# Kernel optimization log

Measured on AMD Instinct MI355X. Metric: run time of the kernel, lower is better.

The kernel has to match this reference:

```python
import jax, jax.numpy as jnp
import numpy as np

B, H, W = 8, 1024, 1024

SOBEL_X = jnp.array([[-1, 0, 1], [-2, 0, 2], [-1, 0, 1]], jnp.float32).reshape(1, 1, 3, 3)
SOBEL_Y = jnp.array([[-1, -2, -1], [0, 0, 0], [1, 2, 1]], jnp.float32).reshape(1, 1, 3, 3)
LAPLACIAN = jnp.array([[0, -1, 0], [-1, 4, -1], [0, -1, 0]], jnp.float32).reshape(1, 1, 3, 3)
TWO_PI = 2.0 * np.pi


def _conv(x, k, pad):
    return jax.lax.conv_general_dilated(
        x, k, window_strides=(1, 1), padding=[(pad, pad), (pad, pad)],
        dimension_numbers=('NCHW', 'OIHW', 'NCHW'))


def _boundary_mask(mask, w):
    ks = 2 * w + 1
    kernel = jnp.ones((1, 1, ks, ks), jnp.float32)
    s = _conv(mask, kernel, w)
    dilated = (s > 0).astype(jnp.float32)
    eroded = (s >= float(ks * ks)).astype(jnp.float32)
    return jnp.clip(dilated - eroded, 0.0, 1.0)


def _elev_grads(e):
    gx = _conv(e, SOBEL_X, 1)
    gy = _conv(e, SOBEL_Y, 1)
    mag = jnp.sqrt(gx * gx + gy * gy + 1e-8)
    dirn = jnp.arctan2(gy, gx + 1e-8)
    curv = _conv(e, LAPLACIAN, 1)
    return mag, dirn, curv


def _high_freq_mask(h, w):
    ii, jj = jnp.meshgrid(jnp.arange(h, dtype=jnp.float32), jnp.arange(w, dtype=jnp.float32), indexing='ij')
    dist = jnp.sqrt((ii - h // 2) ** 2 + (jj - w // 2) ** 2)
    return (dist > min(h, w) * 0.3).astype(jnp.float32).reshape(1, 1, h, w)


def setup_inputs() -> dict:
    key = jax.random.key(0)
    k1, k2, k3 = jax.random.split(key, 3)
    pred = jax.random.normal(k1, (B, 1, H, W), jnp.float32)
    target = jax.random.normal(k2, (B, 1, H, W), jnp.float32)
    mask = jax.random.randint(k3, (B, 1, H, W), 0, 2).astype(jnp.float32)
    return {'pred_elevation': pred, 'target_elevation': target, 'mask': mask}


def reference(pred_elevation, target_elevation, mask):
    # boundary masks for widths 1..3
    bms = [_boundary_mask(mask, w) for w in (1, 2, 3)]

    # ---- gradient continuity loss ----
    p_mag, p_dir, p_curv = _elev_grads(pred_elevation)
    t_mag, t_dir, t_curv = _elev_grads(target_elevation)
    slope_diff = jnp.abs(p_mag - t_mag)
    dir_diff = jnp.abs(p_dir - t_dir)
    dir_diff = jnp.minimum(dir_diff, TWO_PI - dir_diff)
    curv_diff = jnp.abs(p_curv - t_curv)
    grad_loss = 0.0
    for i, bm in enumerate(bms):
        w_sd = 1.0 if i == 0 else 0.5
        w_cv = 2.0 if i == 0 else 1.0
        grad_loss = grad_loss + w_sd * jnp.mean(slope_diff * bm)
        grad_loss = grad_loss + w_sd * jnp.mean(dir_diff * bm)
        grad_loss = grad_loss + w_cv * jnp.mean(curv_diff * bm)
    grad_loss = grad_loss / len(bms)

    # ---- frequency continuity loss ----
    pf = jnp.fft.fft2(pred_elevation)
    tf = jnp.fft.fft2(target_elevation)
    p_magf, t_magf = jnp.abs(pf), jnp.abs(tf)
    p_ph = jnp.arctan2(pf.imag, pf.real)
    t_ph = jnp.arctan2(tf.imag, tf.real)
    hf = _high_freq_mask(H, W)
    mag_loss = jnp.mean((p_magf * hf - t_magf * hf) ** 2)
    d = p_ph - t_ph
    phase_diff = jnp.arctan2(jnp.sin(d), jnp.cos(d))  # wrap to (-pi, pi]
    phase_loss = jnp.mean((phase_diff * hf) ** 2)
    freq_loss = mag_loss + 2.0 * phase_loss

    # ---- smoothness constraint (width_1 only) ----
    kern9 = jnp.ones((1, 1, 3, 3), jnp.float32) / 9.0
    local_mean = _conv(pred_elevation, kern9, 1)
    local_mean_sq = _conv(pred_elevation ** 2, kern9, 1)
    local_var = jnp.clip(local_mean_sq - local_mean ** 2, 1e-8, None)
    local_std = jnp.sqrt(local_var)
    smooth_loss = jnp.mean(local_std * bms[0])

    # ---- slope continuity (width_1 only) ----
    psx = _conv(p_mag, SOBEL_X, 1)
    psy = _conv(p_mag, SOBEL_Y, 1)
    p_change = jnp.sqrt(psx ** 2 + psy ** 2 + 1e-8)
    tsx = _conv(t_mag, SOBEL_X, 1)
    tsy = _conv(t_mag, SOBEL_Y, 1)
    t_change = jnp.sqrt(tsx ** 2 + tsy ** 2 + 1e-8)
    slope_loss = jnp.mean(jnp.abs(p_change - t_change) * bms[0])

    total = 2.0 * grad_loss + 1.5 * freq_loss + 3.0 * smooth_loss + 2.0 * slope_loss
    return (total, grad_loss, freq_loss, smooth_loss, slope_loss)
```

## Files before the change

### kernel.cpp

```cpp
#include <hip/hip_runtime.h>

#define HW 1024
#define TWO_PI_F 6.28318530717958647692f
#define NSLOT 64

typedef float v2f __attribute__((ext_vector_type(2)));
typedef int   i2v __attribute__((ext_vector_type(2)));

__device__ __forceinline__ v2f mkv2(float a, float b){ v2f r; r.x = a; r.y = b; return r; }
__device__ __forceinline__ v2f v2s(float s){ v2f r; r.x = s; r.y = s; return r; }

__device__ __forceinline__ float2 cmulf(float2 a, float2 b){
  return make_float2(a.x*b.x - a.y*b.y, a.x*b.y + a.y*b.x);
}
__device__ __forceinline__ float fsqrt(float x){ return __builtin_amdgcn_sqrtf(x); }

__device__ __forceinline__ float fast_atan2_abs(float ay, float x){
  float ax = fabsf(x);
  float mx = fmaxf(ax, ay), mn = fminf(ax, ay);
  float a  = mn * __builtin_amdgcn_rcpf(fmaxf(mx, 1e-37f));
  float s  = a * a;
  float r  = ((((0.0208351f*s - 0.085133f)*s + 0.180141f)*s - 0.3302995f)*s
              + 0.999866f) * a;
  r = (ay > ax) ? 1.57079632679f - r : r;
  return (x < 0.f) ? 3.14159265359f - r : r;
}

__device__ __forceinline__ float block_reduce_add_f(float v, float* sc){
  int tid = threadIdx.x;
  #pragma unroll
  for (int o = 32; o > 0; o >>= 1) v += __shfl_down(v, o, 64);
  __syncthreads();
  if ((tid & 63) == 0) sc[tid >> 6] = v;
  __syncthreads();
  return sc[0] + sc[1] + sc[2] + sc[3];
}

__global__ void setup_kernel(double* acc, float2* twg){
  int i = threadIdx.x + blockIdx.x * 256;
  if (i < 5 * NSLOT) acc[i] = 0.0;
  if (i < 512){
    float s, c; sincosf(-TWO_PI_F * (float)i * (1.f/1024.f), &s, &c);
    twg[i] = make_float2(c, s);
  }
}

template<int Z0>
__global__ __launch_bounds__(256, 4)
void spatial_kernel(const float* __restrict__ pred, const float* __restrict__ targ,
                    const float* __restrict__ mask, double* __restrict__ acc){
  __shared__ v2f spt[36*44];
  __shared__ v2f pmt[34*35];
  __shared__ unsigned long long mrow[38];
  __shared__ float sc[4];
  float* const smkf = (float*)pmt;

  const int tid = threadIdx.x;
  const int x0 = blockIdx.x << 5, y0 = blockIdx.y << 5;
  const int z = blockIdx.z + Z0;
  const size_t ib = (size_t)z * ((size_t)HW * HW);
  const bool interior = ((unsigned)(blockIdx.x - 1) < 30u) &&
                        ((unsigned)(blockIdx.y - 1) < 30u);

  if (interior){
    const float* pb = pred + ib;
    const float* tb = targ + ib;
    for (int i = tid; i < 360; i += 256){
      int a = i / 10, b = i % 10;
      size_t off = (size_t)(y0 - 2 + a) * HW + (x0 - 4 + 4*b);
      float4 pv = *(const float4*)(pb + off);
      float4 tv = *(const float4*)(tb + off);
      int o = a*44 + 4*b;
      spt[o+0] = mkv2(pv.x, tv.x);
      spt[o+1] = mkv2(pv.y, tv.y);
      spt[o+2] = mkv2(pv.z, tv.z);
      spt[o+3] = mkv2(pv.w, tv.w);
    }
    const float* mb = mask + ib;
    for (int i = tid; i < 380; i += 256){
      int a = i / 10, b = i % 10;
      size_t off = (size_t)(y0 - 3 + a) * HW + (x0 - 4 + 4*b);
      float4 v = *(const float4*)(mb + off);
      int o = a*41 + 4*b;
      smkf[o]=v.x; smkf[o+1]=v.y; smkf[o+2]=v.z; smkf[o+3]=v.w;
    }
  } else {
    for (int i = tid; i < 1296; i += 256){
      int a = i / 36, b = i % 36;
      int gy = y0 - 2 + a, gx = x0 - 2 + b;
      float pv = 0.f, tv = 0.f;
      if ((unsigned)gy < HW && (unsigned)gx < HW){
        size_t idx = ib + (size_t)gy * HW + gx;
        pv = pred[idx]; tv = targ[idx];
      }
      spt[a*44 + b + 2] = mkv2(pv, tv);
    }
    for (int i = tid; i < 1444; i += 256){
      int a = i / 38, b = i % 38;
      int gy = y0 - 3 + a, gx = x0 - 3 + b;
      float v = 0.f;
      if ((unsigned)gy < HW && (unsigned)gx < HW) v = mask[ib + (size_t)gy * HW + gx];
      smkf[a*41 + b + 1] = v;
    }
  }
  __syncthreads();

  {
    const int wv = tid >> 6, lane = tid & 63;
    for (int r = wv; r < 38; r += 4){
      float val = (lane < 38) ? smkf[r*41 + 1 + lane] : 0.f;
      unsigned long long m = __ballot(val > 0.5f);
      if (lane == 0) mrow[r] = m;
    }
  }
  __syncthreads();

  if (interior){
    for (int i = tid; i < 1156; i += 256){
      int iy = i / 34, ix = i % 34;
      int o = iy*44 + ix + 2;
      v2f a00=spt[o],    a01=spt[o+1],  a02=spt[o+2];
      v2f a10=spt[o+44],                a12=spt[o+46];
      v2f a20=spt[o+88], a21=spt[o+89], a22=spt[o+90];
      v2f gx = (a02 + v2s(2.f)*a12 + a22) - (a00 + v2s(2.f)*a10 + a20);
      v2f gy = (a20 + v2s(2.f)*a21 + a22) - (a00 + v2s(2.f)*a01 + a02);
      v2f m2 = gx*gx + gy*gy + v2s(1e-8f);
      pmt[iy*35+ix] = mkv2(fsqrt(m2.x), fsqrt(m2.y));
    }
  } else {
    for (int i = tid; i < 1156; i += 256){
      int iy = i / 34, ix = i % 34;
      int gy = y0 - 1 + iy, gx = x0 - 1 + ix;
      v2f out = v2s(0.f);
      if ((unsigned)gy < HW && (unsigned)gx < HW){
        int o = iy*44 + ix + 2;
        v2f a00=spt[o],    a01=spt[o+1],  a02=spt[o+2];
        v2f a10=spt[o+44],                a12=spt[o+46];
        v2f a20=spt[o+88], a21=spt[o+89], a22=spt[o+90];
        v2f gxv = (a02 + v2s(2.f)*a12 + a22) - (a00 + v2s(2.f)*a10 + a20);
        v2f gyv = (a20 + v2s(2.f)*a21 + a22) - (a00 + v2s(2.f)*a01 + a02);
        v2f m2 = gxv*gxv + gyv*gyv + v2s(1e-8f);
        out = mkv2(fsqrt(m2.x), fsqrt(m2.y));
      }
      pmt[iy*35+ix] = out;
    }
  }
  __syncthreads();

  const int ty = tid >> 5, tx = tid & 31;
  const int r0 = ty << 2;

  int cp[10];
  #pragma unroll
  for (int j = 0; j < 10; j++){
    unsigned w = (unsigned)(mrow[r0 + j] >> tx);
    int c3 = __popc(w & 0x7Fu);
    int c2 = __popc((w >> 1) & 0x1Fu);
    int c1 = __popc((w >> 2) & 0x7u);
    cp[j] = c1 | (c2 << 8) | (c3 << 16);
  }

  v2f PQ[3][3], AB[3][3];
  #pragma unroll
  for (int rr = 0; rr < 2; rr++)
    #pragma unroll
    for (int cc = 0; cc < 3; cc++){
      PQ[rr][cc] = spt[(r0+1+rr)*44 + tx+3+cc];
      AB[rr][cc] = pmt[(r0+rr)*35 + tx+cc];
    }

  v2f wR[6], wA[6];
  float uR[6], qR[6];
  #pragma unroll
  for (int r = 0; r < 2; r++){
    wR[r] = PQ[r][0] + v2s(2.f)*PQ[r][1] + PQ[r][2];
    float p0 = PQ[r][0].x, p1 = PQ[r][1].x, p2 = PQ[r][2].x;
    uR[r] = p0 + p1 + p2;
    qR[r] = fmaf(p0, p0, fmaf(p1, p1, p2*p2));
    wA[r] = AB[r][0] + v2s(2.f)*AB[r][1] + AB[r][2];
  }

  float accg = 0.f, accs = 0.f, accl = 0.f;
  #pragma unroll
  for (int k = 0; k < 4; k++){
    #pragma unroll
    for (int cc = 0; cc < 3; cc++){
      PQ[2][cc] = spt[(r0+k+3)*44 + tx+3+cc];
      AB[2][cc] = pmt[(r0+k+2)*35 + tx+cc];
    }
    {
      wR[k+2] = PQ[2][0] + v2s(2.f)*PQ[2][1] + PQ[2][2];
      float p0 = PQ[2][0].x, p1 = PQ[2][1].x, p2 = PQ[2][2].x;
      uR[k+2] = p0 + p1 + p2;
      qR[k+2] = fmaf(p0, p0, fmaf(p1, p1, p2*p2));
      wA[k+2] = AB[2][0] + v2s(2.f)*AB[2][1] + AB[2][2];
    }

    v2f gxv = (PQ[0][2] + v2s(2.f)*PQ[1][2] + PQ[2][2]) - (PQ[0][0] + v2s(2.f)*PQ[1][0] + PQ[2][0]);
    v2f gyv = wR[k+2] - wR[k];
    v2f cvv = v2s(4.f)*PQ[1][1] - PQ[0][1] - PQ[1][0] - PQ[1][2] - PQ[2][1];

    float sd = fabsf(AB[1][1].x - AB[1][1].y);
    float x1 = gxv.x + 1e-8f, y1 = gyv.x;
    float x2 = gxv.y + 1e-8f, y2 = gyv.y;
    float dd = fast_atan2_abs(fabsf(y1*x2 - x1*y2), x1*x2 + y1*y2);
    float cd = fabsf(cvv.x - cvv.y);

    int s1p = cp[k+2] + cp[k+3] + cp[k+4];
    int s2p = s1p + cp[k+1] + cp[k+5];
    int s3p = s2p + cp[k]   + cp[k+6];
    int s1 = s1p & 0xFF;
    int s2 = (s2p >> 8) & 0xFF;
    int s3 = s3p >> 16;
    float w1 = ((unsigned)(s1 - 1) <  8u) ? 1.f : 0.f;
    float w2 = ((unsigned)(s2 - 1) < 24u) ? 1.f : 0.f;
    float w3 = ((unsigned)(s3 - 1) < 48u) ? 1.f : 0.f;
    float wa = fmaf(0.5f, w2 + w3, w1);

    accg = fmaf(wa, sd + dd + 2.f*cd, accg);

    float s9 = uR[k] + uR[k+1] + uR[k+2];
    float s9q = qR[k] + qR[k+1] + qR[k+2];
    float lm = s9 * (1.f/9.f), lq = s9q * (1.f/9.f);
    accs = fmaf(fsqrt(fmaxf(lq - lm*lm, 1e-8f)), w1, accs);

    v2f px = (AB[0][2] + v2s(2.f)*AB[1][2] + AB[2][2]) - (AB[0][0] + v2s(2.f)*AB[1][0] + AB[2][0]);
    v2f py = wA[k+2] - wA[k];
    v2f ch2 = px*px + py*py + v2s(1e-8f);
    accl = fmaf(fabsf(fsqrt(ch2.x) - fsqrt(ch2.y)), w1, accl);

    if (k < 3){
      #pragma unroll
      for (int cc = 0; cc < 3; cc++){
        PQ[0][cc] = PQ[1][cc]; PQ[1][cc] = PQ[2][cc];
        AB[0][cc] = AB[1][cc]; AB[1][cc] = AB[2][cc];
      }
    }
  }

  float g  = block_reduce_add_f(accg, sc);
  float sm = block_reduce_add_f(accs, sc);
  float sl = block_reduce_add_f(accl, sc);
  if (tid == 0){
    int slot = (blockIdx.x + blockIdx.y * 7 + z * 13) & (NSLOT - 1);
    atomicAdd(&acc[0*NSLOT + slot], (double)g);
    atomicAdd(&acc[1*NSLOT + slot], (double)sm);
    atomicAdd(&acc[2*NSLOT + slot], (double)sl);
  }
}

template<int CTRL>
__device__ __forceinline__ float xordpp(float x){
  int xi = __float_as_int(x);
  return __int_as_float(__builtin_amdgcn_update_dpp(xi, xi, CTRL, 0xF, 0xF, true));
}
__device__ __forceinline__ float xor4v(float x){
  int xi = __float_as_int(x);
  int t1 = __builtin_amdgcn_update_dpp(xi, xi, 0x104, 0xF, 0x5, false);
  int t2 = __builtin_amdgcn_update_dpp(t1, xi, 0x114, 0xF, 0xA, false);
  return __int_as_float(t2);
}

#define FC 0.70710678118654752f
#define FC1 0.92387953251128676f
#define FS1 0.38268343236508977f

__device__ __forceinline__ void bfly(float2& a, float2& b){
  float tx = b.x, ty = b.y;
  b.x = a.x - tx; b.y = a.y - ty;
  a.x += tx;      a.y += ty;
}
__device__ __forceinline__ void cmul_c(float2& b, float wr, float wi){
  float tx = wr*b.x - wi*b.y, ty = wr*b.y + wi*b.x;
  b.x = tx; b.y = ty;
}
__device__ __forceinline__ void rotmi(float2& b){
  float t = b.x; b.x = b.y; b.y = -t;
}

__device__ __forceinline__ void fft16_reg(float2* v){
  float2 y[16];
  y[0]=v[0];  y[1]=v[8];  y[2]=v[4];  y[3]=v[12];
  y[4]=v[2];  y[5]=v[10]; y[6]=v[6];  y[7]=v[14];
  y[8]=v[1];  y[9]=v[9];  y[10]=v[5]; y[11]=v[13];
  y[12]=v[3]; y[13]=v[11];y[14]=v[7]; y[15]=v[15];
  #pragma unroll
  for (int g = 0; g < 8; g++) bfly(y[2*g], y[2*g+1]);
  #pragma unroll
  for (int g = 0; g < 4; g++){
    int b = 4*g;
    bfly(y[b], y[b+2]);
    rotmi(y[b+3]); bfly(y[b+1], y[b+3]);
  }
  #pragma unroll
  for (int g = 0; g < 2; g++){
    int b = 8*g;
    bfly(y[b], y[b+4]);
    cmul_c(y[b+5],  FC, -FC); bfly(y[b+1], y[b+5]);
    rotmi(y[b+6]);            bfly(y[b+2], y[b+6]);
    cmul_c(y[b+7], -FC, -FC); bfly(y[b+3], y[b+7]);
  }
  bfly(y[0], y[8]);
  cmul_c(y[9],   FC1, -FS1); bfly(y[1], y[9]);
  cmul_c(y[10],  FC,  -FC);  bfly(y[2], y[10]);
  cmul_c(y[11],  FS1, -FC1); bfly(y[3], y[11]);
  rotmi(y[12]);              bfly(y[4], y[12]);
  cmul_c(y[13], -FS1, -FC1); bfly(y[5], y[13]);
  cmul_c(y[14], -FC,  -FC);  bfly(y[6], y[14]);
  cmul_c(y[15], -FC1, -FS1); bfly(y[7], y[15]);
  #pragma unroll
  for (int j = 0; j < 16; j++) v[j] = y[j];
}

__device__ __forceinline__ void fft1024_wave(float2* v, int lane ,
                                             const float2* __restrict__ twg){
  const float2 tw1 = twg[(lane & 1) << 8];
  const float2 tw2 = twg[(lane & 3) << 7];
  const float2 tw3 = twg[(lane & 7) << 6];
  const float2 tw4 = twg[(lane & 15) << 5];
  const float2 tw5 = twg[(lane & 31) << 4];
  const float2 wq  = twg[lane];

  {
    const float sgn = (lane & 1) ? -1.f : 1.f;
    #pragma unroll
    for (int j = 0; j < 16; j++){
      i2v px = __builtin_amdgcn_permlane32_swap(__float_as_int(v[j].x), __float_as_int(v[j].x), false, false);
      i2v py = __builtin_amdgcn_permlane32_swap(__float_as_int(v[j].y), __float_as_int(v[j].y), false, false);
      v[j].x = fmaf(sgn, __int_as_float(px.y), __int_as_float(px.x));
      v[j].y = fmaf(sgn, __int_as_float(py.y), __int_as_float(py.x));
    }
  }
  {
    const bool up = (lane & 2) != 0;
    const float ewx = up ? tw1.x : 1.f, ewy = up ? tw1.y : 0.f;
    const float sgn = up ? -1.f : 1.f;
    #pragma unroll
    for (int j = 0; j < 16; j++){
      float tx = ewx*v[j].x - ewy*v[j].y;
      float ty = ewx*v[j].y + ewy*v[j].x;
      i2v px = __builtin_amdgcn_permlane16_swap(__float_as_int(tx), __float_as_int(tx), false, false);
      i2v py = __builtin_amdgcn_permlane16_swap(__float_as_int(ty), __float_as_int(ty), false, false);
      v[j].x = fmaf(sgn, __int_as_float(px.y), __int_as_float(px.x));
      v[j].y = fmaf(sgn, __int_as_float(py.y), __int_as_float(py.x));
    }
  }
  {
    const bool up = (lane & 4) != 0;
    const float ewx = up ? tw2.x : 1.f, ewy = up ? tw2.y : 0.f;
    const float sgn = up ? -1.f : 1.f;
    #pragma unroll
    for (int j = 0; j < 16; j++){
      float tx = ewx*v[j].x - ewy*v[j].y;
      float ty = ewx*v[j].y + ewy*v[j].x;
      v[j].x = fmaf(sgn, tx, xordpp<0x128>(tx));
      v[j].y = fmaf(sgn, ty, xordpp<0x128>(ty));
    }
  }
  {
    const bool up = (lane & 8) != 0;
    const float ewx = up ? tw3.x : 1.f, ewy = up ? tw3.y : 0.f;
    const float sgn = up ? -1.f : 1.f;
    #pragma unroll
    for (int j = 0; j < 16; j++){
      float tx = ewx*v[j].x - ewy*v[j].y;
      float ty = ewx*v[j].y + ewy*v[j].x;
      v[j].x = fmaf(sgn, tx, xor4v(tx));
      v[j].y = fmaf(sgn, ty, xor4v(ty));
    }
  }
  {
    const bool up = (lane & 16) != 0;
    const float ewx = up ? tw4.x : 1.f, ewy = up ? tw4.y : 0.f;
    const float sgn = up ? -1.f : 1.f;
    #pragma unroll
    for (int j = 0; j < 16; j++){
      float tx = ewx*v[j].x - ewy*v[j].y;
      float ty = ewx*v[j].y + ewy*v[j].x;
      v[j].x = fmaf(sgn, tx, xordpp<0x4E>(tx));
      v[j].y = fmaf(sgn, ty, xordpp<0x4E>(ty));
    }
  }
  {
    const bool up = (lane & 32) != 0;
    const float ewx = up ? tw5.x : 1.f, ewy = up ? tw5.y : 0.f;
    const float sgn = up ? -1.f : 1.f;
    #pragma unroll
    for (int j = 0; j < 16; j++){
      float tx = ewx*v[j].x - ewy*v[j].y;
      float ty = ewx*v[j].y + ewy*v[j].x;
      v[j].x = fmaf(sgn, tx, xordpp<0xB1>(tx));
      v[j].y = fmaf(sgn, ty, xordpp<0xB1>(ty));
    }
  }
  float2 w2 = cmulf(wq, wq);
  float2 w3 = cmulf(w2, wq);
  float2 w4 = cmulf(w2, w2);
  float2 w5 = cmulf(w3, w2);
  float2 w6 = cmulf(w3, w3);
  float2 w7 = cmulf(w4, w3);
  float2 w8 = cmulf(w4, w4);
  v[1]  = cmulf(v[1],  wq);
  v[2]  = cmulf(v[2],  w2);
  v[3]  = cmulf(v[3],  w3);
  v[4]  = cmulf(v[4],  w4);
  v[5]  = cmulf(v[5],  w5);
  v[6]  = cmulf(v[6],  w6);
  v[7]  = cmulf(v[7],  w7);
  v[8]  = cmulf(v[8],  w8);
  v[9]  = cmulf(cmulf(v[9],  w8), wq);
  v[10] = cmulf(cmulf(v[10], w8), w2);
  v[11] = cmulf(cmulf(v[11], w8), w3);
  v[12] = cmulf(cmulf(v[12], w8), w4);
  v[13] = cmulf(cmulf(v[13], w8), w5);
  v[14] = cmulf(cmulf(v[14], w8), w6);
  v[15] = cmulf(cmulf(v[15], w8), w7);
  fft16_reg(v);
}

__global__ __launch_bounds__(512, 2)
void fft_rows_t_kernel(const float* __restrict__ pred, const float* __restrict__ targ,
                       float2* __restrict__ Zt, const float2* __restrict__ twg){
  __shared__ float2 tile[8][64][9];
  const int tid = threadIdx.x;
  const int lane = tid & 63;
  const int w = tid >> 6;
  const int y0 = blockIdx.x << 3;
  const size_t ibase = ((size_t)blockIdx.y * HW + (y0 + w)) * HW;
  const int rb = __brev(lane) >> 26;
  const float4* p4 = (const float4*)(pred + ibase);
  const float4* t4 = (const float4*)(targ + ibase);
  float2 v[16];
  #pragma unroll
  for (int m = 0; m < 4; m++){
    float4 a = p4[4*lane + m];
    float4 b = t4[4*lane + m];
    v[4*m+0] = make_float2(a.x, b.x);
    v[4*m+1] = make_float2(a.y, b.y);
    v[4*m+2] = make_float2(a.z, b.z);
    v[4*m+3] = make_float2(a.w, b.w);
  }
  fft1024_wave(v, rb, twg);
  float2* zb = Zt + (size_t)blockIdx.y * HW * HW + (size_t)blockIdx.x * 8192;
  const int yl = tid & 7, kl = tid >> 3;
  #pragma unroll
  for (int jb = 0; jb < 2; jb++){
    __syncthreads();
    #pragma unroll
    for (int jj = 0; jj < 8; jj++) tile[jj][lane][w] = v[8*jb + jj];
    __syncthreads();
    #pragma unroll
    for (int jj = 0; jj < 8; jj++){
      int k = ((jb << 3) + jj) * 64 + kl;
      zb[k * 8 + yl] = tile[jj][kl][yl];
    }
  }
}

__device__ __forceinline__ void freq_contrib(float2 Zk, float2 Zm, int k1, int k2,
                                             float& ms, float& ps){
  int di = k1 - 512, dj = k2 - 512;
  if (di*di + dj*dj < 94372) return;
  float pr = 0.5f*(Zk.x + Zm.x);
  float pi = 0.5f*(Zk.y - Zm.y);
  float tr = 0.5f*(Zk.y + Zm.y);
  float ti = 0.5f*(Zm.x - Zk.x);
  float p2 = pr*pr + pi*pi;
  float t2 = tr*tr + ti*ti;
  ms += p2 + t2 - 2.f*fsqrt(p2*t2);
  float re = pr*tr + pi*ti;
  float im = pi*tr - pr*ti;
  float pd = fast_atan2_abs(fabsf(im), re);
  ps += pd*pd;
}

__global__ __launch_bounds__(256, 2)
void fft_cols2_kernel(const float2* __restrict__ Z, const float2* __restrict__ twg,
                      double* __restrict__ acc){
  __shared__ float2 ex[4][1024];
  const int lane = threadIdx.x & 63;
  const int w = threadIdx.x >> 6;
  const int p = 2 * blockIdx.x + (w >> 1);
  const bool valid = (p <= 512);
  const int r_spec = (w & 1) ? ((1024 - p) & 1023) : p;
  const int rr = (r_spec & 0x3C0) | (__brev(r_spec & 63) >> 26);
  const float2* base = Z + (size_t)blockIdx.y * HW * HW;
  const int bl = __brev(lane) >> 26;

  float2 v[16];
  if (valid){
    const float4* f4 = (const float4*)base;
    #pragma unroll
    for (int s = 0; s < 2; s++){
      size_t o = (size_t)(2*lane + s) * 4096 + (size_t)rr * 4;
      #pragma unroll
      for (int q = 0; q < 4; q++){
        float4 x = f4[o + q];
        v[8*s + 2*q]     = make_float2(x.x, x.y);
        v[8*s + 2*q + 1] = make_float2(x.z, x.w);
      }
    }
    fft1024_wave(v, bl, twg);
    #pragma unroll
    for (int j = 0; j < 16; j++) ex[w][bl + (j << 6)] = v[j];
  }
  __syncthreads();
  if (!valid) return;
  const bool self = (p == 0) || (p == 512);
  if ((w & 1) && self) return;

  const float2* pb = ex[w ^ 1];
  float ms = 0.f, ps = 0.f;
  #pragma unroll
  for (int j = 0; j < 16; j++){
    int k = bl + (j << 6);
    float2 zm = pb[(1024 - k) & 1023];
    freq_contrib(v[j], zm, k, r_spec, ms, ps);
  }
  #pragma unroll
  for (int o = 32; o > 0; o >>= 1){
    ms += __shfl_down(ms, o, 64);
    ps += __shfl_down(ps, o, 64);
  }
  if (lane == 0){
    int slot = (r_spec + blockIdx.y * 11) & (NSLOT - 1);
    atomicAdd(&acc[3*NSLOT + slot], (double)ms);
    atomicAdd(&acc[4*NSLOT + slot], (double)ps);
  }
}

__global__ void finalize_kernel(const double* __restrict__ acc, float* __restrict__ out){
  const int t = threadIdx.x;
  double v[5];
  #pragma unroll
  for (int s = 0; s < 5; s++) v[s] = acc[s*NSLOT + t];
  #pragma unroll
  for (int o = 32; o > 0; o >>= 1)
    #pragma unroll
    for (int s = 0; s < 5; s++) v[s] += __shfl_down(v[s], o, 64);
  if (t == 0){
    const double inv = 1.0 / 8388608.0;
    double grad   = v[0] * inv / 3.0;
    double smooth = v[1] * inv;
    double slope  = v[2] * inv;
    double freq   = (v[3] + 2.0 * v[4]) * inv;
    double total  = 2.0*grad + 1.5*freq + 3.0*smooth + 2.0*slope;
    out[0] = (float)total;
    out[1] = (float)grad;
    out[2] = (float)freq;
    out[3] = (float)smooth;
    out[4] = (float)slope;
  }
}

extern "C" void kernel_launch(void* const* d_in, const int* in_sizes, int n_in,
                              void* d_out, int out_size, void* d_ws, size_t ws_size,
                              hipStream_t stream){
  const float* pred = (const float*)d_in[0];
  const float* targ = (const float*)d_in[1];
  const float* mask = (const float*)d_in[2];
  double* acc  = (double*)d_ws;
  float2* twg  = (float2*)((char*)d_ws + 4096);
  float2* Z    = (float2*)((char*)d_ws + 8192);

  setup_kernel<<<2, 256, 0, stream>>>(acc, twg);
  spatial_kernel<0><<<dim3(32, 32, 4), 256, 0, stream>>>(pred, targ, mask, acc);
  spatial_kernel<4><<<dim3(32, 32, 4), 256, 0, stream>>>(pred, targ, mask, acc);
  fft_rows_t_kernel<<<dim3(128, 8), 512, 0, stream>>>(pred, targ, Z, twg);
  fft_cols2_kernel<<<dim3(257, 8), 256, 0, stream>>>(Z, twg, acc);
  finalize_kernel<<<1, 64, 0, stream>>>(acc, (float*)d_out);
}
```

Measured before the change: 241.1 us.

## Drop setup kernel, compute twiddles inline, merge spatial launches

Removes the setup kernel: the accumulators are now zeroed with hipMemsetAsync and the FFT twiddles are computed per lane with sincosf instead of read from a global table. The two spatial_kernel launches (batches 0-3 and 4-7) become one launch over all 8 batches. The aim is fewer launches and fewer inter-kernel gaps, at the cost of extra transcendental math in each FFT wave.

```diff
diff --git a/kernel.cpp b/kernel.cpp
--- a/kernel.cpp
+++ b/kernel.cpp
@@ -36,16 +36,6 @@
   return sc[0] + sc[1] + sc[2] + sc[3];
 }
 
-__global__ void setup_kernel(double* acc, float2* twg){
-  int i = threadIdx.x + blockIdx.x * 256;
-  if (i < 5 * NSLOT) acc[i] = 0.0;
-  if (i < 512){
-    float s, c; sincosf(-TWO_PI_F * (float)i * (1.f/1024.f), &s, &c);
-    twg[i] = make_float2(c, s);
-  }
-}
-
-template<int Z0>
 __global__ __launch_bounds__(256, 4)
 void spatial_kernel(const float* __restrict__ pred, const float* __restrict__ targ,
                     const float* __restrict__ mask, double* __restrict__ acc){
@@ -57,7 +47,7 @@
 
   const int tid = threadIdx.x;
   const int x0 = blockIdx.x << 5, y0 = blockIdx.y << 5;
-  const int z = blockIdx.z + Z0;
+  const int z = blockIdx.z;
   const size_t ib = (size_t)z * ((size_t)HW * HW);
   const bool interior = ((unsigned)(blockIdx.x - 1) < 30u) &&
                         ((unsigned)(blockIdx.y - 1) < 30u);
@@ -312,14 +302,19 @@
   for (int j = 0; j < 16; j++) v[j] = y[j];
 }
 
-__device__ __forceinline__ void fft1024_wave(float2* v, int lane ,
-                                             const float2* __restrict__ twg){
-  const float2 tw1 = twg[(lane & 1) << 8];
-  const float2 tw2 = twg[(lane & 3) << 7];
-  const float2 tw3 = twg[(lane & 7) << 6];
-  const float2 tw4 = twg[(lane & 15) << 5];
-  const float2 tw5 = twg[(lane & 31) << 4];
-  const float2 wq  = twg[lane];
+__device__ __forceinline__ float2 twf(int idx){
+  float s, c;
+  sincosf(-TWO_PI_F * (float)idx * (1.f/1024.f), &s, &c);
+  return make_float2(c, s);
+}
+
+__device__ __forceinline__ void fft1024_wave(float2* v, int lane ){
+  const float2 tw1 = twf((lane & 1) << 8);
+  const float2 tw2 = twf((lane & 3) << 7);
+  const float2 tw3 = twf((lane & 7) << 6);
+  const float2 tw4 = twf((lane & 15) << 5);
+  const float2 tw5 = twf((lane & 31) << 4);
+  const float2 wq  = twf(lane);
 
   {
     const float sgn = (lane & 1) ? -1.f : 1.f;
@@ -420,7 +415,7 @@
 
 __global__ __launch_bounds__(512, 2)
 void fft_rows_t_kernel(const float* __restrict__ pred, const float* __restrict__ targ,
-                       float2* __restrict__ Zt, const float2* __restrict__ twg){
+                       float2* __restrict__ Zt){
   __shared__ float2 tile[8][64][9];
   const int tid = threadIdx.x;
   const int lane = tid & 63;
@@ -440,7 +435,7 @@
     v[4*m+2] = make_float2(a.z, b.z);
     v[4*m+3] = make_float2(a.w, b.w);
   }
-  fft1024_wave(v, rb, twg);
+  fft1024_wave(v, rb);
   float2* zb = Zt + (size_t)blockIdx.y * HW * HW + (size_t)blockIdx.x * 8192;
   const int yl = tid & 7, kl = tid >> 3;
   #pragma unroll
@@ -475,8 +470,7 @@
 }
 
 __global__ __launch_bounds__(256, 2)
-void fft_cols2_kernel(const float2* __restrict__ Z, const float2* __restrict__ twg,
-                      double* __restrict__ acc){
+void fft_cols2_kernel(const float2* __restrict__ Z, double* __restrict__ acc){
   __shared__ float2 ex[4][1024];
   const int lane = threadIdx.x & 63;
   const int w = threadIdx.x >> 6;
@@ -500,7 +494,7 @@
         v[8*s + 2*q + 1] = make_float2(x.z, x.w);
       }
     }
-    fft1024_wave(v, bl, twg);
+    fft1024_wave(v, bl);
     #pragma unroll
     for (int j = 0; j < 16; j++) ex[w][bl + (j << 6)] = v[j];
   }
@@ -560,13 +554,11 @@
   const float* targ = (const float*)d_in[1];
   const float* mask = (const float*)d_in[2];
   double* acc  = (double*)d_ws;
-  float2* twg  = (float2*)((char*)d_ws + 4096);
   float2* Z    = (float2*)((char*)d_ws + 8192);
 
-  setup_kernel<<<2, 256, 0, stream>>>(acc, twg);
-  spatial_kernel<0><<<dim3(32, 32, 4), 256, 0, stream>>>(pred, targ, mask, acc);
-  spatial_kernel<4><<<dim3(32, 32, 4), 256, 0, stream>>>(pred, targ, mask, acc);
-  fft_rows_t_kernel<<<dim3(128, 8), 512, 0, stream>>>(pred, targ, Z, twg);
-  fft_cols2_kernel<<<dim3(257, 8), 256, 0, stream>>>(Z, twg, acc);
+  hipMemsetAsync(acc, 0, 5 * NSLOT * sizeof(double), stream);
+  spatial_kernel<<<dim3(32, 32, 8), 256, 0, stream>>>(pred, targ, mask, acc);
+  fft_rows_t_kernel<<<dim3(128, 8), 512, 0, stream>>>(pred, targ, Z);
+  fft_cols2_kernel<<<dim3(257, 8), 256, 0, stream>>>(Z, acc);
   finalize_kernel<<<1, 64, 0, stream>>>(acc, (float*)d_out);
 }
```

Measured after the change: 231.9 us. 3.8% less time.
